# Performance work log

Hardware: AMD Instinct MI355X
Metric: run time of the kernel (lower is better)

## Reference

```python
import jax, jax.numpy as jnp
import numpy as np

N_USERS = 50000
N_ENTITIES = 100000
D = 64
R = 16
E_UI = 1500000
E_KG = 100000


def setup_inputs() -> dict:
    key = jax.random.key(0)
    ks = jax.random.split(key, 7)
    s = 1.0 / np.sqrt(D)  # ~xavier scale
    return {
        "user_indices": jnp.arange(N_USERS, dtype=jnp.int32),
        "item_indices": jnp.arange(N_ENTITIES, dtype=jnp.int32),
        "edge_index_ui": jax.random.randint(ks[0], (2, E_UI), 0, N_USERS + N_ENTITIES, dtype=jnp.int32),
        "edge_index_kg": jax.random.randint(ks[1], (2, E_KG), 0, N_ENTITIES, dtype=jnp.int32),
        "edge_type_kg": jax.random.randint(ks[2], (E_KG,), 0, R, dtype=jnp.int32),
        "user_table": (jax.random.normal(ks[3], (N_USERS, D)) * s).astype(jnp.float32),
        "entity_table": (jax.random.normal(ks[4], (N_ENTITIES, D)) * s).astype(jnp.float32),
        "W": (jax.random.normal(ks[5], (D, D)) * s).astype(jnp.float32),
        "W_r": (jax.random.normal(ks[6], (R, D, D)) * s).astype(jnp.float32),
    }


def _kgat_layer(x, edge_index, W, W_r, edge_type=None):
    # PyG aggr='add', flow source_to_target: x_j = x[src], x_i = x[dst], scatter to dst
    src, dst = edge_index[0], edge_index[1]
    x_j = x[src]  # [E, D]
    x_i = x[dst]  # [E, D]
    if edge_type is None:
        x_j_t = x_j @ W  # [E, D]
    else:
        # per-edge relation-specific transform: bmm(x_j[:,None,:], W_r[edge_type])
        x_j_t = jnp.einsum('ed,edo->eo', x_j, W_r[edge_type])
    # bi-interaction attention
    x_i_t = x_i @ W
    logits = jnp.sum(x_i_t * x_j_t, axis=1, keepdims=True)  # [E, 1]
    logits = jax.nn.leaky_relu(logits, negative_slope=0.2)
    scores = jax.nn.softmax(logits, axis=0)  # GLOBAL softmax over all edges (as in source)
    msg = scores * x_j_t  # [E, D]
    return jax.ops.segment_sum(msg, dst, num_segments=x.shape[0])


def reference(user_indices, item_indices, edge_index_ui, edge_index_kg, edge_type_kg,
              user_table, entity_table, W, W_r):
    user_embeds = user_table[user_indices]      # [n_users, D]
    item_embeds = entity_table[item_indices]    # [n_entities, D]
    x = jnp.concatenate([user_embeds, item_embeds], axis=0)
    # single layer (layer_dims = [embed_dim])
    x_ui = _kgat_layer(x, edge_index_ui, W, W_r, edge_type=None)
    x_kg = _kgat_layer(item_embeds, edge_index_kg, W, W_r, edge_type=edge_type_kg)
    x = x.at[N_USERS:].add(x_kg)  # faithful to source: overwritten by next line (dead store)
    x = jax.nn.relu(x_ui)
    # F.dropout(training=False) -> identity in eval mode
    return (x[:N_USERS], x[N_USERS:])
```

## Files before the change

### kernel.cpp

```cpp
#include <hip/hip_runtime.h>

#define NU 50000
#define NE 100000
#define NN 150000
#define DD 64
#define EUI 1500000

#define TPB 256
#define NBLK 2048
#define NSB 586
#define NS23 147
#define NXB 2344
#define NXH (NXB + NBLK)
#define NBF2 9375
#define NSC 9375

#define XWB_OFF    0ull
#define PD_OFF     4800000ull
#define SSRC_OFF   6300000ull
#define CNT_OFF    7800000ull
#define ROWPTR_OFF 7950000ull
#define BSUM_OFF   8100004ull
#define PSUM_OFF   8100590ull
#define SCAL_OFF   8110000ull

__device__ __forceinline__ unsigned bfpack(float a, float b) {
  unsigned ua = __float_as_uint(a);
  ua = (ua + 0x7fffu + ((ua >> 16) & 1u)) >> 16;
  unsigned ub = __float_as_uint(b);
  ub = (ub + 0x7fffu + ((ub >> 16) & 1u)) & 0xffff0000u;
  return (ua & 0xffffu) | ub;
}

template <int CTRL>
__device__ __forceinline__ float dpp_add(float x) {
  int y = __builtin_amdgcn_update_dpp(0, __float_as_int(x), CTRL, 0xF, 0xF, false);
  return x + __int_as_float(y);
}
__device__ __forceinline__ float row16_sum(float x) {
  x = dpp_add<0x124>(x);
  x = dpp_add<0x128>(x);
  x = dpp_add<0xB1>(x);
  x = dpp_add<0x4E>(x);
  return x;
}

__global__ __launch_bounds__(TPB) void k_xw_hist(const int* __restrict__ uidx,
                                                 const int* __restrict__ iidx,
                                                 const float* __restrict__ ut,
                                                 const float* __restrict__ et,
                                                 const float* __restrict__ W,
                                                 unsigned* __restrict__ xwb,
                                                 const int* __restrict__ ei,
                                                 int* __restrict__ cnt,
                                                 unsigned* __restrict__ pd) {
  const int bi = blockIdx.x;
  int idx;
  bool hist;
  if (bi < 2 * NBLK) { hist = (bi & 1); idx = bi >> 1; }
  else               { hist = false;    idx = bi - NBLK; }

  if (hist) {
    for (int e = idx * TPB + threadIdx.x; e < EUI; e += NBLK * TPB) {
      const int dst = ei[EUI + e];
      const unsigned r = (unsigned)atomicAdd(&cnt[dst], 1);
      pd[e] = (r << 18) | (unsigned)dst;
    }
    return;
  }

  __shared__ float Ws[DD * DD];
  __shared__ float Xs[64 * 68];
  const int t = threadIdx.x;
  {
    const float4* W4 = (const float4*)W;
    float4* Ws4 = (float4*)Ws;
#pragma unroll
    for (int i = 0; i < 4; ++i) Ws4[t + i * TPB] = W4[t + i * TPB];
  }
  {
    const int rl = t >> 2, ch = t & 3;
    int row = idx * 64 + rl;
    if (row >= NN) row = NN - 1;
    const float4* s4 = (const float4*)((row < NU)
        ? ut + (size_t)uidx[row] * DD
        : et + (size_t)iidx[row - NU] * DD);
    float4* x4 = (float4*)(Xs + rl * 68);
#pragma unroll
    for (int j = 0; j < 4; ++j) x4[ch + 4 * j] = s4[ch + 4 * j];
  }
  __syncthreads();
  const int q = t & 15, g = t >> 4;
  float4 acc[4] = {{0,0,0,0},{0,0,0,0},{0,0,0,0},{0,0,0,0}};
  const float* __restrict__ wsq = Ws + 4 * q;
  const float* __restrict__ xsg = Xs + (4 * g) * 68;
#pragma unroll 1
  for (int kc = 0; kc < 16; ++kc) {
    const float4 w0 = *(const float4*)(wsq + (4 * kc + 0) * DD);
    const float4 w1 = *(const float4*)(wsq + (4 * kc + 1) * DD);
    const float4 w2 = *(const float4*)(wsq + (4 * kc + 2) * DD);
    const float4 w3 = *(const float4*)(wsq + (4 * kc + 3) * DD);
#pragma unroll
    for (int i = 0; i < 4; ++i) {
      const float4 x = *(const float4*)(xsg + i * 68 + 4 * kc);
      acc[i].x = fmaf(x.x, w0.x, acc[i].x);
      acc[i].y = fmaf(x.x, w0.y, acc[i].y);
      acc[i].z = fmaf(x.x, w0.z, acc[i].z);
      acc[i].w = fmaf(x.x, w0.w, acc[i].w);
      acc[i].x = fmaf(x.y, w1.x, acc[i].x);
      acc[i].y = fmaf(x.y, w1.y, acc[i].y);
      acc[i].z = fmaf(x.y, w1.z, acc[i].z);
      acc[i].w = fmaf(x.y, w1.w, acc[i].w);
      acc[i].x = fmaf(x.z, w2.x, acc[i].x);
      acc[i].y = fmaf(x.z, w2.y, acc[i].y);
      acc[i].z = fmaf(x.z, w2.z, acc[i].z);
      acc[i].w = fmaf(x.z, w2.w, acc[i].w);
      acc[i].x = fmaf(x.w, w3.x, acc[i].x);
      acc[i].y = fmaf(x.w, w3.y, acc[i].y);
      acc[i].z = fmaf(x.w, w3.z, acc[i].z);
      acc[i].w = fmaf(x.w, w3.w, acc[i].w);
    }
  }
#pragma unroll
  for (int i = 0; i < 4; ++i) {
    const int row = idx * 64 + 4 * g + i;
    if (row < NN) {
      uint2 p;
      p.x = bfpack(acc[i].x, acc[i].y);
      p.y = bfpack(acc[i].z, acc[i].w);
      ((uint2*)(xwb + (size_t)row * 32))[q] = p;
    }
  }
}

__global__ __launch_bounds__(TPB) void k_scan1(int* __restrict__ cnt,
                                               int* __restrict__ bsum) {
  __shared__ int sh[TPB];
  const int t = threadIdx.x;
  const int i = blockIdx.x * TPB + t;
  const int v = (i < NN) ? cnt[i] : 0;
  sh[t] = v;
  __syncthreads();
#pragma unroll
  for (int off = 1; off < TPB; off <<= 1) {
    int add = (t >= off) ? sh[t - off] : 0;
    __syncthreads();
    sh[t] += add;
    __syncthreads();
  }
  if (i < NN) cnt[i] = sh[t] - v;
  if (t == TPB - 1) bsum[blockIdx.x] = sh[t];
}

__global__ __launch_bounds__(1024) void k_scan23(const int* __restrict__ excl,
                                                 const int* __restrict__ bsum,
                                                 int* __restrict__ rowptr) {
  __shared__ int sh[1024];
  const int t = threadIdx.x;
  const int v = (t < NSB) ? bsum[t] : 0;
  sh[t] = v;
  __syncthreads();
#pragma unroll
  for (int off = 1; off < 1024; off <<= 1) {
    int add = (t >= off) ? sh[t - off] : 0;
    __syncthreads();
    sh[t] += add;
    __syncthreads();
  }
  const int boff = sh[t] - v;
  __syncthreads();
  sh[t] = boff;
  __syncthreads();
  const int i = blockIdx.x * 1024 + t;
  if (i < NN) rowptr[i] = excl[i] + sh[i >> 8];
  if (i == 0) rowptr[NN] = EUI;
}

__global__ __launch_bounds__(TPB) void k_fill(const int* __restrict__ ei,
                                              const unsigned* __restrict__ pd,
                                              const int* __restrict__ rowptr,
                                              int* __restrict__ ssrc) {
  for (int e = blockIdx.x * TPB + threadIdx.x; e < EUI; e += gridDim.x * TPB) {
    const unsigned p = pd[e];
    ssrc[rowptr[p & 0x3ffffu] + (int)(p >> 18)] = ei[e];
  }
}

__global__ __launch_bounds__(TPB) void k_fused(const int* __restrict__ rowptr,
                                               const int* __restrict__ ssrc,
                                               const unsigned* __restrict__ xwb,
                                               float* __restrict__ out,
                                               float* __restrict__ psum) {
  const int lane = threadIdx.x & 63;
  const int wv = threadIdx.x >> 6;
  const int sub = lane >> 4;
  const int q = lane & 15;
  const int n = blockIdx.x * 16 + wv * 4 + sub;
  const uint2* __restrict__ x2 = (const uint2*)xwb;
  const uint2 dv = x2[(size_t)n * 16 + q];
  const float vd0 = __uint_as_float(dv.x << 16);
  const float vd1 = __uint_as_float(dv.x & 0xffff0000u);
  const float vd2 = __uint_as_float(dv.y << 16);
  const float vd3 = __uint_as_float(dv.y & 0xffff0000u);
  const int b = rowptr[n], en = rowptr[n + 1];
  float a0 = 0.f, a1 = 0.f, a2 = 0.f, a3 = 0.f, wacc = 0.f;
  for (int it = b;; it += 2) {
    const bool act0 = it < en;
    if (!__any(act0)) break;
    const bool act1 = it + 1 < en;
    const int s0 = ssrc[act0 ? it : b];
    const int s1 = ssrc[act1 ? it + 1 : b];
    const uint2 sv0 = x2[(size_t)s0 * 16 + q];
    const uint2 sv1 = x2[(size_t)s1 * 16 + q];
    const float u0 = __uint_as_float(sv0.x << 16);
    const float u1 = __uint_as_float(sv0.x & 0xffff0000u);
    const float u2 = __uint_as_float(sv0.y << 16);
    const float u3 = __uint_as_float(sv0.y & 0xffff0000u);
    const float t0 = __uint_as_float(sv1.x << 16);
    const float t1 = __uint_as_float(sv1.x & 0xffff0000u);
    const float t2 = __uint_as_float(sv1.y << 16);
    const float t3 = __uint_as_float(sv1.y & 0xffff0000u);
    float p0 = vd0 * u0;
    p0 = fmaf(vd1, u1, p0);
    p0 = fmaf(vd2, u2, p0);
    p0 = fmaf(vd3, u3, p0);
    float p1 = vd0 * t0;
    p1 = fmaf(vd1, t1, p1);
    p1 = fmaf(vd2, t2, p1);
    p1 = fmaf(vd3, t3, p1);
    p0 = row16_sum(p0);
    p1 = row16_sum(p1);
    const float l0 = (p0 > 0.f) ? p0 : 0.2f * p0;
    const float l1 = (p1 > 0.f) ? p1 : 0.2f * p1;
    float w0 = __expf(l0);
    float w1 = __expf(l1);
    if (!act0) w0 = 0.f;
    if (!act1) w1 = 0.f;
    a0 = fmaf(w0, u0, a0);
    a1 = fmaf(w0, u1, a1);
    a2 = fmaf(w0, u2, a2);
    a3 = fmaf(w0, u3, a3);
    a0 = fmaf(w1, t0, a0);
    a1 = fmaf(w1, t1, a1);
    a2 = fmaf(w1, t2, a2);
    a3 = fmaf(w1, t3, a3);
    wacc += w0 + w1;
  }
  float4 r = {a0, a1, a2, a3};
  ((float4*)(out + (size_t)n * DD))[q] = r;
  __shared__ float sm[16];
  if (q == 0) sm[wv * 4 + sub] = wacc;
  __syncthreads();
  if (threadIdx.x == 0) {
    float s = 0.f;
#pragma unroll
    for (int i = 0; i < 16; ++i) s += sm[i];
    psum[blockIdx.x] = s;
  }
}

__global__ __launch_bounds__(TPB) void k_rsum(const float* __restrict__ psum,
                                              float* __restrict__ scal) {
  float s = 0.f;
  for (int i = threadIdx.x; i < NBF2; i += TPB) s += psum[i];
#pragma unroll
  for (int off = 32; off; off >>= 1) s += __shfl_xor(s, off, 64);
  __shared__ float sm[4];
  if ((threadIdx.x & 63) == 0) sm[threadIdx.x >> 6] = s;
  __syncthreads();
  if (threadIdx.x == 0) scal[0] = sm[0] + sm[1] + sm[2] + sm[3];
}

__global__ __launch_bounds__(TPB) void k_scale(float* __restrict__ out,
                                               const float* __restrict__ scal) {
  const float inv = 1.0f / scal[0];
  const int i = blockIdx.x * TPB + threadIdx.x;
  float4* o4 = (float4*)out;
  float4 v = o4[i];
  v.x = fmaxf(v.x * inv, 0.f);
  v.y = fmaxf(v.y * inv, 0.f);
  v.z = fmaxf(v.z * inv, 0.f);
  v.w = fmaxf(v.w * inv, 0.f);
  o4[i] = v;
}

extern "C" void kernel_launch(void* const* d_in, const int* in_sizes, int n_in,
                              void* d_out, int out_size, void* d_ws, size_t ws_size,
                              hipStream_t stream) {
  const int* uidx = (const int*)d_in[0];
  const int* iidx = (const int*)d_in[1];
  const int* ei_ui = (const int*)d_in[2];
  const float* ut = (const float*)d_in[5];
  const float* et = (const float*)d_in[6];
  const float* W = (const float*)d_in[7];

  float* out = (float*)d_out;
  float* ws = (float*)d_ws;
  unsigned* xwb = (unsigned*)(ws + XWB_OFF);
  unsigned* pd = (unsigned*)(ws + PD_OFF);
  int* ssrc = (int*)(ws + SSRC_OFF);
  int* cnt = (int*)(ws + CNT_OFF);
  int* rowptr = (int*)(ws + ROWPTR_OFF);
  int* bsum = (int*)(ws + BSUM_OFF);
  float* psum = ws + PSUM_OFF;
  float* scal = ws + SCAL_OFF;

  (void)hipMemsetAsync(cnt, 0, (size_t)NN * sizeof(int), stream);

  k_xw_hist<<<NXH, TPB, 0, stream>>>(uidx, iidx, ut, et, W, xwb, ei_ui, cnt, pd);
  k_scan1<<<NSB, TPB, 0, stream>>>(cnt, bsum);
  k_scan23<<<NS23, 1024, 0, stream>>>(cnt, bsum, rowptr);
  k_fill<<<NBLK, TPB, 0, stream>>>(ei_ui, pd, rowptr, ssrc);
  k_fused<<<NBF2, TPB, 0, stream>>>(rowptr, ssrc, xwb, out, psum);
  k_rsum<<<1, TPB, 0, stream>>>(psum, scal);
  k_scale<<<NSC, TPB, 0, stream>>>(out, scal);
}
```

Before: 279.9 us.

## Privatize edge-destination histogram per XCD to localize atomics

The destination-count histogram is split into eight per-XCD planes indexed by the hardware XCC id. Atomics become workgroup-scoped on an XCD-local plane, which keeps contention inside one L2. Scan and fill are extended to fold the planes into per-plane offsets, and the XCD id is packed into the per-edge record. This adds a larger memset, extra plane traffic in the scan kernels, and a reliance on the XCC_ID register and workgroup-scope atomics staying correct across CUs.

```diff
diff --git a/kernel.cpp b/kernel.cpp
--- a/kernel.cpp
+++ b/kernel.cpp
@@ -18,7 +18,7 @@
 #define XWB_OFF    0ull
 #define PD_OFF     4800000ull
 #define SSRC_OFF   6300000ull
-#define CNT_OFF    7800000ull
+#define TEXCL_OFF  7800000ull
 #define ROWPTR_OFF 7950000ull
 #define BSUM_OFF   8100004ull
 #define PSUM_OFF   8100590ull
@@ -30,6 +30,12 @@
   unsigned ub = __float_as_uint(b);
   ub = (ub + 0x7fffu + ((ub >> 16) & 1u)) & 0xffff0000u;
   return (ua & 0xffffu) | ub;
+}
+
+__device__ __forceinline__ unsigned xcc_id() {
+  unsigned x;
+  asm volatile("s_getreg_b32 %0, hwreg(HW_REG_XCC_ID)" : "=s"(x));
+  return x & 7u;
 }
 
 template <int CTRL>
@@ -52,7 +58,7 @@
                                                  const float* __restrict__ W,
                                                  unsigned* __restrict__ xwb,
                                                  const int* __restrict__ ei,
-                                                 int* __restrict__ cnt,
+                                                 unsigned* __restrict__ cnt8,
                                                  unsigned* __restrict__ pd) {
   const int bi = blockIdx.x;
   int idx;
@@ -61,10 +67,15 @@
   else               { hist = false;    idx = bi - NBLK; }
 
   if (hist) {
+    const unsigned xcd = xcc_id();
+    unsigned* __restrict__ plane = cnt8 + (size_t)xcd * NN;
+    const unsigned xtag = xcd << 29;
     for (int e = idx * TPB + threadIdx.x; e < EUI; e += NBLK * TPB) {
       const int dst = ei[EUI + e];
-      const unsigned r = (unsigned)atomicAdd(&cnt[dst], 1);
-      pd[e] = (r << 18) | (unsigned)dst;
+      const unsigned r = __hip_atomic_fetch_add(&plane[dst], 1u,
+                                                __ATOMIC_RELAXED,
+                                                __HIP_MEMORY_SCOPE_WORKGROUP);
+      pd[e] = xtag | (r << 18) | (unsigned)dst;
     }
     return;
   }
@@ -133,13 +144,24 @@
   }
 }
 
-__global__ __launch_bounds__(TPB) void k_scan1(int* __restrict__ cnt,
+__global__ __launch_bounds__(TPB) void k_scan1(unsigned* __restrict__ cnt8,
+                                               int* __restrict__ texcl,
                                                int* __restrict__ bsum) {
   __shared__ int sh[TPB];
   const int t = threadIdx.x;
   const int i = blockIdx.x * TPB + t;
-  const int v = (i < NN) ? cnt[i] : 0;
-  sh[t] = v;
+  int tot = 0;
+  if (i < NN) {
+    unsigned run = 0;
+#pragma unroll
+    for (int x = 0; x < 8; ++x) {
+      const unsigned v = cnt8[(size_t)x * NN + i];
+      cnt8[(size_t)x * NN + i] = run;
+      run += v;
+    }
+    tot = (int)run;
+  }
+  sh[t] = tot;
   __syncthreads();
 #pragma unroll
   for (int off = 1; off < TPB; off <<= 1) {
@@ -148,13 +170,14 @@
     sh[t] += add;
     __syncthreads();
   }
-  if (i < NN) cnt[i] = sh[t] - v;
+  if (i < NN) texcl[i] = sh[t] - tot;
   if (t == TPB - 1) bsum[blockIdx.x] = sh[t];
 }
 
 __global__ __launch_bounds__(1024) void k_scan23(const int* __restrict__ excl,
                                                  const int* __restrict__ bsum,
-                                                 int* __restrict__ rowptr) {
+                                                 int* __restrict__ rowptr,
+                                                 unsigned* __restrict__ cnt8) {
   __shared__ int sh[1024];
   const int t = threadIdx.x;
   const int v = (t < NSB) ? bsum[t] : 0;
@@ -172,17 +195,25 @@
   sh[t] = boff;
   __syncthreads();
   const int i = blockIdx.x * 1024 + t;
-  if (i < NN) rowptr[i] = excl[i] + sh[i >> 8];
+  if (i < NN) {
+    const int rp = excl[i] + sh[i >> 8];
+    rowptr[i] = rp;
+#pragma unroll
+    for (int x = 0; x < 8; ++x) cnt8[(size_t)x * NN + i] += (unsigned)rp;
+  }
   if (i == 0) rowptr[NN] = EUI;
 }
 
 __global__ __launch_bounds__(TPB) void k_fill(const int* __restrict__ ei,
                                               const unsigned* __restrict__ pd,
-                                              const int* __restrict__ rowptr,
+                                              const unsigned* __restrict__ cnt8,
                                               int* __restrict__ ssrc) {
   for (int e = blockIdx.x * TPB + threadIdx.x; e < EUI; e += gridDim.x * TPB) {
     const unsigned p = pd[e];
-    ssrc[rowptr[p & 0x3ffffu] + (int)(p >> 18)] = ei[e];
+    const unsigned dst = p & 0x3ffffu;
+    const unsigned xcd = p >> 29;
+    const int rank = (int)((p >> 18) & 0x7ffu);
+    ssrc[cnt8[(size_t)xcd * NN + dst] + rank] = ei[e];
   }
 }
 
@@ -299,18 +330,19 @@
   unsigned* xwb = (unsigned*)(ws + XWB_OFF);
   unsigned* pd = (unsigned*)(ws + PD_OFF);
   int* ssrc = (int*)(ws + SSRC_OFF);
-  int* cnt = (int*)(ws + CNT_OFF);
+  int* texcl = (int*)(ws + TEXCL_OFF);
   int* rowptr = (int*)(ws + ROWPTR_OFF);
   int* bsum = (int*)(ws + BSUM_OFF);
   float* psum = ws + PSUM_OFF;
   float* scal = ws + SCAL_OFF;
-
-  (void)hipMemsetAsync(cnt, 0, (size_t)NN * sizeof(int), stream);
-
-  k_xw_hist<<<NXH, TPB, 0, stream>>>(uidx, iidx, ut, et, W, xwb, ei_ui, cnt, pd);
-  k_scan1<<<NSB, TPB, 0, stream>>>(cnt, bsum);
-  k_scan23<<<NS23, 1024, 0, stream>>>(cnt, bsum, rowptr);
-  k_fill<<<NBLK, TPB, 0, stream>>>(ei_ui, pd, rowptr, ssrc);
+  unsigned* cnt8 = (unsigned*)d_out;
+
+  (void)hipMemsetAsync(cnt8, 0, (size_t)8 * NN * sizeof(unsigned), stream);
+
+  k_xw_hist<<<NXH, TPB, 0, stream>>>(uidx, iidx, ut, et, W, xwb, ei_ui, cnt8, pd);
+  k_scan1<<<NSB, TPB, 0, stream>>>(cnt8, texcl, bsum);
+  k_scan23<<<NS23, 1024, 0, stream>>>(texcl, bsum, rowptr, cnt8);
+  k_fill<<<NBLK, TPB, 0, stream>>>(ei_ui, pd, cnt8, ssrc);
   k_fused<<<NBF2, TPB, 0, stream>>>(rowptr, ssrc, xwb, out, psum);
   k_rsum<<<1, TPB, 0, stream>>>(psum, scal);
   k_scale<<<NSC, TPB, 0, stream>>>(out, scal);
```

Result: no change. 285.4 us (+2.0%).
